# Kernel tuning notes

Hardware: AMD Instinct MI355X
Metric: run time of the kernel (lower is better)

## Reference

```python
import jax, jax.numpy as jnp
import numpy as np
from jax import lax

T, B, DX, H, DZ = 512, 64, 128, 256, 64
W_SCALE = 0.05


def setup_inputs() -> dict:
    key = jax.random.key(0)
    ks = jax.random.split(key, 16)
    r = lambda k, shape, s=W_SCALE: jax.random.normal(k, shape, dtype=jnp.float32) * s
    return {
        "X": jax.random.normal(ks[0], (T, B, DX), dtype=jnp.float32),
        "Wih_f": r(ks[1], (H, DX)), "Whh_f": r(ks[2], (H, H)),
        "bih_f": r(ks[3], (H,)), "bhh_f": r(ks[4], (H,)),
        "Wih_b": r(ks[5], (H, DX)), "Whh_b": r(ks[6], (H, H)),
        "bih_b": r(ks[7], (H,)), "bhh_b": r(ks[8], (H,)),
        "Wt": r(ks[9], (H, DZ)), "bt": r(ks[10], (H,)),
        "Wmu": r(ks[11], (DZ, H)), "bmu": r(ks[12], (DZ,)),
        "Wsig": r(ks[13], (DZ, H)), "bsig": r(ks[14], (DZ,)),
        "eps": jax.random.normal(ks[15], (T, B, DZ), dtype=jnp.float32),
    }


def _rnn_dir(X, Wih, Whh, bih, bhh):
    # Elman RNN (tanh): h_t = tanh(x_t Wih^T + bih + h_{t-1} Whh^T + bhh)
    xproj = jnp.einsum('tbd,hd->tbh', X, Wih) + bih + bhh  # big GEMM hoisted out of scan

    def step(h, xp):
        h = jnp.tanh(xp + h @ Whh.T)
        return h, h

    h0 = jnp.zeros((X.shape[1], Whh.shape[0]), dtype=X.dtype)
    _, hs = lax.scan(step, h0, xproj)
    return hs  # [T,B,H]


def reference(X, Wih_f, Whh_f, bih_f, bhh_f, Wih_b, Whh_b, bih_b, bhh_b,
              Wt, bt, Wmu, bmu, Wsig, bsig, eps):
    h_left = _rnn_dir(X, Wih_f, Whh_f, bih_f, bhh_f)
    h_right = _rnn_dir(X[::-1], Wih_b, Whh_b, bih_b, bhh_b)[::-1]

    def step(z_prev, inputs):
        hl, hr, eps_t = inputs
        tmp = jnp.tanh(z_prev @ Wt.T + bt)           # transition_net
        h_t = (tmp + hl + hr) * (1.0 / 3.0)
        mu = h_t @ Wmu.T + bmu
        std = jax.nn.softplus(h_t @ Wsig.T + bsig)
        z = mu + std * eps_t                         # reparameterization
        return z, (z, mu, std)

    z0 = jnp.zeros((X.shape[1], Wt.shape[1]), dtype=X.dtype)
    _, (z, mu, std) = lax.scan(step, z0, (h_left, h_right, eps))
    # stack outputs {z_post, mu_post, std_post} into one array [3,T,B,DZ]
    return jnp.stack([z, mu, std])
```

## Files before the change

kernel.cpp:

```cpp
#include <hip/hip_runtime.h>

#define TT 512
#define DXX 128
#define HH 256
#define DZZ 64

typedef __attribute__((ext_vector_type(8))) short short8;
typedef __attribute__((ext_vector_type(4))) float f32x4;

#define DEV static __device__ __forceinline__
#define MFMA(a,b,c) __builtin_amdgcn_mfma_f32_16x16x32_bf16((a),(b),(c),0,0,0)

DEV unsigned short f2bf(float f){
  unsigned u = __builtin_bit_cast(unsigned, f);
  u += 0x7FFFu + ((u >> 16) & 1u);
  return (unsigned short)(u >> 16);
}
DEV unsigned pack2(float lo, float hi){
  return (unsigned)f2bf(lo) | ((unsigned)f2bf(hi) << 16);
}
DEV float bfLO(unsigned u){ return __builtin_bit_cast(float, u << 16); }
DEV float bfHI(unsigned u){ return __builtin_bit_cast(float, u & 0xffff0000u); }
DEV float ftanh(float x){
  float a = fabsf(x);
  float e = __expf(-2.f * a);
  float r = __builtin_amdgcn_rcpf(1.f + e);
  float t = (1.f - e) * r;
  return copysignf(t, x);
}
DEV float fsoftplus(float x){
  float e = __expf(fminf(x, 20.f));
  float s = __logf(1.f + e);
  return (x > 20.f) ? x : s;
}
DEV void barrier_l(){
  asm volatile("s_waitcnt lgkmcnt(0)\n\ts_barrier" ::: "memory");
}


__global__ __launch_bounds__(256, 2) void phaseA(
    const float* __restrict__ X,
    const float* __restrict__ WihF, const float* __restrict__ bihF, const float* __restrict__ bhhF,
    const float* __restrict__ WihB, const float* __restrict__ bihB, const float* __restrict__ bhhB,
    unsigned short* __restrict__ xpF)
{
  const int bid = blockIdx.x;
  const int d = bid >> 9, s = bid & 511;
  const int ts = d ? (TT - 1 - s) : s;
  const float* W  = d ? WihB : WihF;
  const float* bi = d ? bihB : bihF;
  const float* bh = d ? bhhB : bhhF;

  const int tid = threadIdx.x, q = tid >> 6, l = tid & 63;
  const int l15 = l & 15, l4 = l >> 4;

  short8 wf[4][4];
  f32x4 bias[4];
  #pragma unroll
  for (int ni = 0; ni < 4; ++ni){
    int n = 64*q + 16*ni + l15;
    #pragma unroll
    for (int ks = 0; ks < 4; ++ks){
      const float* p = W + (size_t)n * DXX + ks*32 + l4*8;
      short8 v;
      #pragma unroll
      for (int i = 0; i < 8; ++i) v[i] = (short)f2bf(p[i]);
      wf[ni][ks] = v;
    }
    int n0 = 64*q + 16*ni + 4*l4;
    float4 b1 = *(const float4*)(bi + n0);
    float4 b2 = *(const float4*)(bh + n0);
    bias[ni][0]=b1.x+b2.x; bias[ni][1]=b1.y+b2.y; bias[ni][2]=b1.z+b2.z; bias[ni][3]=b1.w+b2.w;
  }

  #pragma unroll
  for (int bq = 0; bq < 4; ++bq){
    const float* xr = X + ((size_t)ts * 64 + 16*bq + l15) * DXX;
    short8 xf[4];
    #pragma unroll
    for (int ks = 0; ks < 4; ++ks){
      const float* p = xr + ks*32 + l4*8;
      short8 v;
      #pragma unroll
      for (int i = 0; i < 8; ++i) v[i] = (short)f2bf(p[i]);
      xf[ks] = v;
    }
    f32x4 acc[4];
    #pragma unroll
    for (int ni = 0; ni < 4; ++ni) acc[ni] = MFMA(wf[ni][0], xf[0], bias[ni]);
    #pragma unroll
    for (int ks = 1; ks < 4; ++ks)
      #pragma unroll
      for (int ni = 0; ni < 4; ++ni)
        acc[ni] = MFMA(wf[ni][ks], xf[ks], acc[ni]);

    unsigned wd[8];
    #pragma unroll
    for (int ni = 0; ni < 4; ++ni){
      wd[ni*2]   = pack2(acc[ni][0], acc[ni][1]);
      wd[ni*2+1] = pack2(acc[ni][2], acc[ni][3]);
    }
    unsigned short* dst = xpF + ((((size_t)d*TT + s)*4 + bq)*4 + q)*1024 + (size_t)l*16;
    uint4 o0 = {wd[0], wd[1], wd[2], wd[3]};
    uint4 o1 = {wd[4], wd[5], wd[6], wd[7]};
    ((uint4*)dst)[0] = o0;
    ((uint4*)dst)[1] = o1;
  }
}

__global__ __launch_bounds__(512, 1) void phaseB(
    const float* __restrict__ WhhF, const float* __restrict__ WhhB,
    const unsigned short* __restrict__ xpF, unsigned short* __restrict__ hF)
{
  const int dir = blockIdx.x >> 2, bq = blockIdx.x & 3;
  const float* Whh = dir ? WhhB : WhhF;
  const int tid = threadIdx.x, w = tid >> 6, l = tid & 63;
  const bool comp = (w < 4);
  const int q = w & 3;
  const int l15 = l & 15, l4 = l >> 4;
  const int swz = (l15 & 7) << 3;
  const int rbase = l15 * 256;

  __shared__ __attribute__((aligned(16))) unsigned short hbuf[2][4096];
  __shared__ __attribute__((aligned(16))) unsigned short hres[2][4096];

  short8 wf[4][8];
  if (comp){
    #pragma unroll
    for (int ni = 0; ni < 4; ++ni){
      int n = 64*q + 16*ni + l15;
      #pragma unroll
      for (int ks = 0; ks < 8; ++ks){
        const float* p = Whh + (size_t)n * HH + ks*32 + l4*8;
        short8 v;
        #pragma unroll
        for (int i = 0; i < 8; ++i) v[i] = (short)f2bf(p[i]);
        wf[ni][ks] = v;
      }
    }
  }
  for (int i = tid; i < 2048; i += 512) ((unsigned*)hbuf[0])[i] = 0u;

  const size_t strideS = 16384;
  const size_t laneOff = (size_t)bq*4096 + (size_t)q*1024 + (size_t)l*16;
  const unsigned short* xpP = xpF + (size_t)dir*TT*strideS + laneOff;
  unsigned short* hD = hF + (size_t)dir*TT*strideS + laneOff;

  uint4 xqA0, xqA1, xqB0, xqB1;
  if (comp){
    const uint4* p0 = (const uint4*)xpP;             xqA0 = p0[0]; xqA1 = p0[1];
    const uint4* p1 = (const uint4*)(xpP + strideS); xqB0 = p1[0]; xqB1 = p1[1];
  }
  __syncthreads();

  auto bstep = [&](int s, uint4& XQ0, uint4& XQ1){
    if (comp){
      const unsigned short* RD = hbuf[s & 1];
      unsigned short* WR = hbuf[(s & 1) ^ 1];
      short8 b[8];
      #pragma unroll
      for (int ks = 0; ks < 8; ++ks)
        b[ks] = *(const short8*)(RD + ((rbase + ks*32 + l4*8) ^ swz));
      f32x4 accE[4], accO[4];
      {
        unsigned W8[8] = {XQ0.x, XQ0.y, XQ0.z, XQ0.w, XQ1.x, XQ1.y, XQ1.z, XQ1.w};
        #pragma unroll
        for (int ni = 0; ni < 4; ++ni){
          accE[ni][0] = bfLO(W8[ni*2]);   accE[ni][1] = bfHI(W8[ni*2]);
          accE[ni][2] = bfLO(W8[ni*2+1]); accE[ni][3] = bfHI(W8[ni*2+1]);
          accO[ni][0] = 0.f; accO[ni][1] = 0.f; accO[ni][2] = 0.f; accO[ni][3] = 0.f;
        }
      }
      {
        int sn = (s + 2 < TT) ? s + 2 : TT - 1;
        const uint4* src = (const uint4*)(xpP + (size_t)sn * strideS);
        XQ0 = src[0]; XQ1 = src[1];
      }
      #pragma unroll
      for (int ks = 0; ks < 8; ks += 2){
        #pragma unroll
        for (int ni = 0; ni < 4; ++ni){
          accE[ni] = MFMA(wf[ni][ks],   b[ks],   accE[ni]);
          accO[ni] = MFMA(wf[ni][ks+1], b[ks+1], accO[ni]);
        }
      }
      unsigned wd[8];
      #pragma unroll
      for (int ni = 0; ni < 4; ++ni){
        float t0 = ftanh(accE[ni][0] + accO[ni][0]);
        float t1 = ftanh(accE[ni][1] + accO[ni][1]);
        float t2 = ftanh(accE[ni][2] + accO[ni][2]);
        float t3 = ftanh(accE[ni][3] + accO[ni][3]);
        unsigned lo = pack2(t0, t1), hi = pack2(t2, t3);
        wd[ni*2] = lo; wd[ni*2+1] = hi;
        int ea = rbase + ((64*q + 16*ni + 4*l4) ^ swz);
        uint2 v; v.x = lo; v.y = hi;
        *(uint2*)(WR + ea) = v;
      }
      {
        unsigned short* st = hres[s & 1] + q*1024 + l*16;
        uint4 o0 = {wd[0], wd[1], wd[2], wd[3]};
        uint4 o1 = {wd[4], wd[5], wd[6], wd[7]};
        ((uint4*)st)[0] = o0;
        ((uint4*)st)[1] = o1;
      }
    } else {
      int sg = (s > 0) ? s - 1 : 0;
      const unsigned short* src = hres[(s & 1) ^ 1] + q*1024 + l*16;
      uint4 p0 = ((const uint4*)src)[0];
      uint4 p1 = ((const uint4*)src)[1];
      size_t off = (size_t)(dir ? (TT - 1 - sg) : sg) * strideS;
      *(uint4*)(hD + off)     = p0;
      *(uint4*)(hD + off + 8) = p1;
    }
    barrier_l();
  };

  for (int s = 0; s < TT; s += 2){
    bstep(s,     xqA0, xqA1);
    bstep(s + 1, xqB0, xqB1);
  }
  if (!comp){
    const unsigned short* src = hres[1] + q*1024 + l*16;
    uint4 p0 = ((const uint4*)src)[0];
    uint4 p1 = ((const uint4*)src)[1];
    size_t off = (size_t)(dir ? 0 : (TT - 1)) * strideS;
    *(uint4*)(hD + off)     = p0;
    *(uint4*)(hD + off + 8) = p1;
  }
}

__global__ __launch_bounds__(256, 2) void phaseP(
    const float* __restrict__ Wmu, const float* __restrict__ bmu,
    const float* __restrict__ Wsig,const float* __restrict__ bsig,
    const unsigned short* __restrict__ hF, float* __restrict__ MS)
{
  const int bid = blockIdx.x;
  const int t = bid >> 2, bq = bid & 3;
  const int tid = threadIdx.x, q = tid >> 6, l = tid & 63;
  const int l15 = l & 15, l4 = l >> 4;
  const int swz = (l15 & 7) << 3;
  const int rbase = l15 * 256;

  __shared__ __attribute__((aligned(16))) unsigned short hbuf[4096];

  short8 wm[8], wsg[8];
  {
    int r = 16*q + l15;
    #pragma unroll
    for (int ks = 0; ks < 8; ++ks){
      const float* pm = Wmu  + (size_t)r * HH + ks*32 + l4*8;
      const float* ps = Wsig + (size_t)r * HH + ks*32 + l4*8;
      short8 vm, vs;
      #pragma unroll
      for (int i = 0; i < 8; ++i){
        vm[i] = (short)f2bf(pm[i] * (1.f/3.f));
        vs[i] = (short)f2bf(ps[i] * (1.f/3.f));
      }
      wm[ks] = vm; wsg[ks] = vs;
    }
  }
  f32x4 bm4, bs4;
  {
    float4 a = *(const float4*)(bmu  + 16*q + 4*l4);
    float4 b = *(const float4*)(bsig + 16*q + 4*l4);
    bm4[0]=a.x; bm4[1]=a.y; bm4[2]=a.z; bm4[3]=a.w;
    bs4[0]=b.x; bs4[1]=b.y; bs4[2]=b.z; bs4[3]=b.w;
  }

  const size_t strideS = 16384;
  const size_t laneOff = (size_t)bq*4096 + (size_t)q*1024 + (size_t)l*16;
  const unsigned short* hl = hF + (size_t)t*strideS + laneOff;
  const unsigned short* hr = hl + (size_t)TT*strideS;
  {
    uint4 a0 = ((const uint4*)hl)[0], a1 = ((const uint4*)hl)[1];
    uint4 b0 = ((const uint4*)hr)[0], b1 = ((const uint4*)hr)[1];
    unsigned HL[8] = {a0.x,a0.y,a0.z,a0.w,a1.x,a1.y,a1.z,a1.w};
    unsigned HR[8] = {b0.x,b0.y,b0.z,b0.w,b1.x,b1.y,b1.z,b1.w};
    #pragma unroll
    for (int ni = 0; ni < 4; ++ni){
      float h0 = bfLO(HL[ni*2])   + bfLO(HR[ni*2]);
      float h1 = bfHI(HL[ni*2])   + bfHI(HR[ni*2]);
      float h2 = bfLO(HL[ni*2+1]) + bfLO(HR[ni*2+1]);
      float h3 = bfHI(HL[ni*2+1]) + bfHI(HR[ni*2+1]);
      int ea = rbase + ((64*q + 16*ni + 4*l4) ^ swz);
      uint2 v; v.x = pack2(h0, h1); v.y = pack2(h2, h3);
      *(uint2*)(hbuf + ea) = v;
    }
  }
  __syncthreads();

  short8 hb[8];
  #pragma unroll
  for (int ks = 0; ks < 8; ++ks)
    hb[ks] = *(const short8*)(hbuf + ((rbase + ks*32 + l4*8) ^ swz));
  const f32x4 zero4 = {0.f,0.f,0.f,0.f};
  f32x4 am0 = MFMA(wm[0],  hb[0], bm4);
  f32x4 as0 = MFMA(wsg[0], hb[0], bs4);
  f32x4 am1 = MFMA(wm[4],  hb[4], zero4);
  f32x4 as1 = MFMA(wsg[4], hb[4], zero4);
  #pragma unroll
  for (int ks = 1; ks < 4; ++ks){
    am0 = MFMA(wm[ks],    hb[ks],   am0);
    as0 = MFMA(wsg[ks],   hb[ks],   as0);
    am1 = MFMA(wm[ks+4],  hb[ks+4], am1);
    as1 = MFMA(wsg[ks+4], hb[ks+4], as1);
  }
  f32x4 mu = am0 + am1;
  f32x4 sg = as0 + as1;
  float* dst = MS + ((((size_t)t*4 + bq)*4 + q)*64 + (size_t)l)*8;
  *(float4*)dst       = *(float4*)&mu;
  *(float4*)(dst + 4) = *(float4*)&sg;
}

__global__ __launch_bounds__(512, 1) void phaseC(
    const float* __restrict__ Wt,  const float* __restrict__ bt,
    const float* __restrict__ Wmu, const float* __restrict__ Wsig,
    const float* __restrict__ eps, const float* __restrict__ MS,
    float* __restrict__ out)
{
  const int bq = blockIdx.x;
  const int tid = threadIdx.x, w = tid >> 6, l = tid & 63;
  const bool comp = (w < 4);
  const int q = w & 3;
  const int l15 = l & 15, l4 = l >> 4;
  const int swz = (l15 & 7) << 3;
  const int rbase = l15 * 256;
  const int zrbase = l15 * 64;

  __shared__ __attribute__((aligned(16))) unsigned short zbuf[1024];
  __shared__ __attribute__((aligned(16))) unsigned short ubuf[4096];
  __shared__ __attribute__((aligned(16))) float res[3072];

  short8 wtf[4][2]; f32x4 btb[4];
  short8 wm[8], wsg[8];
  if (comp){
    #pragma unroll
    for (int ni = 0; ni < 4; ++ni){
      int n = 64*q + 16*ni + l15;
      #pragma unroll
      for (int ks = 0; ks < 2; ++ks){
        const float* p = Wt + (size_t)n * DZZ + ks*32 + l4*8;
        short8 v;
        #pragma unroll
        for (int i = 0; i < 8; ++i) v[i] = (short)f2bf(p[i]);
        wtf[ni][ks] = v;
      }
      float4 b4 = *(const float4*)(bt + 64*q + 16*ni + 4*l4);
      btb[ni][0]=b4.x; btb[ni][1]=b4.y; btb[ni][2]=b4.z; btb[ni][3]=b4.w;
    }
    int r = 16*q + l15;
    #pragma unroll
    for (int ks = 0; ks < 8; ++ks){
      const float* pm = Wmu  + (size_t)r * HH + ks*32 + l4*8;
      const float* ps = Wsig + (size_t)r * HH + ks*32 + l4*8;
      short8 vm, vs;
      #pragma unroll
      for (int i = 0; i < 8; ++i){
        vm[i] = (short)f2bf(pm[i] * (1.f/3.f));
        vs[i] = (short)f2bf(ps[i] * (1.f/3.f));
      }
      wm[ks] = vm; wsg[ks] = vs;
    }
  }
  if (tid < 512) ((unsigned*)zbuf)[tid] = 0u;

  const float* msP = MS + (((size_t)bq*4 + q)*64 + (size_t)l)*8;
  const float* eP  = eps + ((size_t)(16*bq + l15))*64 + 16*q + 4*l4;
  const int resoff = (q*64 + l)*12;
  const size_t TBZ = (size_t)TT * 64 * 64;
  const f32x4 zero4 = {0.f,0.f,0.f,0.f};

  f32x4 MPa, SPa, EFa, MPb, SPb, EFb;
  if (comp){
    float4 m0 = *(const float4*)(msP);         float4 s0 = *(const float4*)(msP + 4);
    float4 m1 = *(const float4*)(msP + 8192);  float4 s1 = *(const float4*)(msP + 8192 + 4);
    float4 e0 = *(const float4*)(eP);
    float4 e1 = *(const float4*)(eP + 4096);
    MPa[0]=m0.x;MPa[1]=m0.y;MPa[2]=m0.z;MPa[3]=m0.w;
    SPa[0]=s0.x;SPa[1]=s0.y;SPa[2]=s0.z;SPa[3]=s0.w;
    MPb[0]=m1.x;MPb[1]=m1.y;MPb[2]=m1.z;MPb[3]=m1.w;
    SPb[0]=s1.x;SPb[1]=s1.y;SPb[2]=s1.z;SPb[3]=s1.w;
    EFa[0]=e0.x;EFa[1]=e0.y;EFa[2]=e0.z;EFa[3]=e0.w;
    EFb[0]=e1.x;EFb[1]=e1.y;EFb[2]=e1.z;EFb[3]=e1.w;
  }
  __syncthreads();

  auto cstep = [&](int t, f32x4& MP, f32x4& SP, f32x4& EF){
    if (comp){
      short8 zb0 = *(const short8*)(zbuf + ((zrbase +  0 + l4*8) ^ swz));
      short8 zb1 = *(const short8*)(zbuf + ((zrbase + 32 + l4*8) ^ swz));
      f32x4 at[4];
      #pragma unroll
      for (int ni = 0; ni < 4; ++ni) at[ni] = MFMA(wtf[ni][0], zb0, btb[ni]);
      #pragma unroll
      for (int ni = 0; ni < 4; ++ni) at[ni] = MFMA(wtf[ni][1], zb1, at[ni]);
      #pragma unroll
      for (int ni = 0; ni < 4; ++ni){
        float u0 = ftanh(at[ni][0]), u1 = ftanh(at[ni][1]);
        float u2 = ftanh(at[ni][2]), u3 = ftanh(at[ni][3]);
        int ea = rbase + ((64*q + 16*ni + 4*l4) ^ swz);
        uint2 v; v.x = pack2(u0, u1); v.y = pack2(u2, u3);
        *(uint2*)(ubuf + ea) = v;
      }
    } else {
      int tp = (t > 0) ? t - 1 : 0;
      const float* rs = res + resoff;
      float4 vz = *(const float4*)(rs);
      float4 vm = *(const float4*)(rs + 4);
      float4 vs = *(const float4*)(rs + 8);
      size_t ob = ((size_t)tp*64 + 16*bq + l15)*64 + 16*q + 4*l4;
      *(float4*)(out + ob)         = vz;
      *(float4*)(out + TBZ + ob)   = vm;
      *(float4*)(out + 2*TBZ + ob) = vs;
    }
    barrier_l();

    if (comp){
      short8 hb[8];
      #pragma unroll
      for (int ks = 0; ks < 8; ++ks)
        hb[ks] = *(const short8*)(ubuf + ((rbase + ks*32 + l4*8) ^ swz));
      f32x4 am0 = MFMA(wm[0],  hb[0], MP);
      f32x4 as0 = MFMA(wsg[0], hb[0], SP);
      f32x4 am1 = MFMA(wm[4],  hb[4], zero4);
      f32x4 as1 = MFMA(wsg[4], hb[4], zero4);
      #pragma unroll
      for (int ks = 1; ks < 4; ++ks){
        am0 = MFMA(wm[ks],    hb[ks],   am0);
        as0 = MFMA(wsg[ks],   hb[ks],   as0);
        am1 = MFMA(wm[ks+4],  hb[ks+4], am1);
        as1 = MFMA(wsg[ks+4], hb[ks+4], as1);
      }
      f32x4 mu = am0 + am1;
      f32x4 sg = as0 + as1;
      f32x4 dz, dsp;
      #pragma unroll
      for (int reg = 0; reg < 4; ++reg){
        float sp = fsoftplus(sg[reg]);
        dz[reg] = __builtin_fmaf(sp, EF[reg], mu[reg]);
        dsp[reg] = sp;
      }
      {
        int zea = zrbase + ((16*q + 4*l4) ^ swz);
        uint2 v; v.x = pack2(dz[0], dz[1]); v.y = pack2(dz[2], dz[3]);
        *(uint2*)(zbuf + zea) = v;
      }
      {
        float* rw = res + resoff;
        *(float4*)(rw)     = *(float4*)&dz;
        *(float4*)(rw + 4) = *(float4*)&mu;
        *(float4*)(rw + 8) = *(float4*)&dsp;
      }
      {
        int tn = (t + 2 < TT) ? t + 2 : TT - 1;
        float4 m = *(const float4*)(msP + (size_t)tn*8192);
        float4 s = *(const float4*)(msP + (size_t)tn*8192 + 4);
        float4 e = *(const float4*)(eP + (size_t)tn*4096);
        MP[0]=m.x;MP[1]=m.y;MP[2]=m.z;MP[3]=m.w;
        SP[0]=s.x;SP[1]=s.y;SP[2]=s.z;SP[3]=s.w;
        EF[0]=e.x;EF[1]=e.y;EF[2]=e.z;EF[3]=e.w;
      }
    }
    barrier_l();
  };

  for (int t = 0; t < TT; t += 2){
    cstep(t,     MPa, SPa, EFa);
    cstep(t + 1, MPb, SPb, EFb);
  }
  if (!comp){
    const float* rs = res + resoff;
    float4 vz = *(const float4*)(rs);
    float4 vm = *(const float4*)(rs + 4);
    float4 vs = *(const float4*)(rs + 8);
    size_t ob = ((size_t)(TT-1)*64 + 16*bq + l15)*64 + 16*q + 4*l4;
    *(float4*)(out + ob)         = vz;
    *(float4*)(out + TBZ + ob)   = vm;
    *(float4*)(out + 2*TBZ + ob) = vs;
  }
}

extern "C" void kernel_launch(void* const* d_in, const int* in_sizes, int n_in,
                              void* d_out, int out_size, void* d_ws, size_t ws_size,
                              hipStream_t stream)
{
  const float* X      = (const float*)d_in[0];
  const float* Wih_f  = (const float*)d_in[1];
  const float* Whh_f  = (const float*)d_in[2];
  const float* bih_f  = (const float*)d_in[3];
  const float* bhh_f  = (const float*)d_in[4];
  const float* Wih_b  = (const float*)d_in[5];
  const float* Whh_b  = (const float*)d_in[6];
  const float* bih_b  = (const float*)d_in[7];
  const float* bhh_b  = (const float*)d_in[8];
  const float* Wt     = (const float*)d_in[9];
  const float* bt     = (const float*)d_in[10];
  const float* Wmu    = (const float*)d_in[11];
  const float* bmu    = (const float*)d_in[12];
  const float* Wsig   = (const float*)d_in[13];
  const float* bsig   = (const float*)d_in[14];
  const float* eps    = (const float*)d_in[15];

  unsigned short* xpF = (unsigned short*)d_ws;
  unsigned short* hF  = xpF + (size_t)2 * TT * 16384;
  float* MS = (float*)d_ws;

  phaseA<<<dim3(1024), dim3(256), 0, stream>>>(X, Wih_f, bih_f, bhh_f, Wih_b, bih_b, bhh_b, xpF);
  phaseB<<<dim3(8), dim3(512), 0, stream>>>(Whh_f, Whh_b, xpF, hF);
  phaseP<<<dim3(2048), dim3(256), 0, stream>>>(Wmu, bmu, Wsig, bsig, hF, MS);
  phaseC<<<dim3(4), dim3(512), 0, stream>>>(Wt, bt, Wmu, Wsig, eps, MS, (float*)d_out);
}
```

Measured before the change: 1.155 ms.

## Drop writer warps; pack two independent recurrences per block and simplify tanh

In the two serial-recurrence kernels, the dedicated writer waves are removed. Compute waves now store their results straight to global memory, and each 512-thread block runs two independent groups (the two directions in phaseB, two batch quarters in phaseC), which halves the grid size. tanh is rewritten as 1-2/(1+exp2(2x·log2e)), and bf16 packing uses the hardware-friendly __float22bfloat162_rn intrinsic. The cost is that global stores now sit on the critical path of each step, groups are coupled through shared barriers, and the new tanh form may overflow to inf for large inputs, though it still evaluates correctly.

```diff
diff --git a/kernel.cpp b/kernel.cpp
--- a/kernel.cpp
+++ b/kernel.cpp
@@ -1,4 +1,5 @@
 #include <hip/hip_runtime.h>
+#include <hip/hip_bf16.h>
 
 #define TT 512
 #define DXX 128
@@ -17,16 +18,16 @@
   return (unsigned short)(u >> 16);
 }
 DEV unsigned pack2(float lo, float hi){
-  return (unsigned)f2bf(lo) | ((unsigned)f2bf(hi) << 16);
+  __hip_bfloat162 v = __float22bfloat162_rn(float2{lo, hi});
+  unsigned r; __builtin_memcpy(&r, &v, 4);
+  return r;
 }
 DEV float bfLO(unsigned u){ return __builtin_bit_cast(float, u << 16); }
 DEV float bfHI(unsigned u){ return __builtin_bit_cast(float, u & 0xffff0000u); }
 DEV float ftanh(float x){
-  float a = fabsf(x);
-  float e = __expf(-2.f * a);
+  float e = exp2f(x * 2.885390082f);
   float r = __builtin_amdgcn_rcpf(1.f + e);
-  float t = (1.f - e) * r;
-  return copysignf(t, x);
+  return __builtin_fmaf(-2.f, r, 1.f);
 }
 DEV float fsoftplus(float x){
   float e = __expf(fminf(x, 20.f));
@@ -112,106 +113,94 @@
     const float* __restrict__ WhhF, const float* __restrict__ WhhB,
     const unsigned short* __restrict__ xpF, unsigned short* __restrict__ hF)
 {
-  const int dir = blockIdx.x >> 2, bq = blockIdx.x & 3;
+  const int bq = blockIdx.x;
+  const int tid = threadIdx.x, w = tid >> 6, l = tid & 63;
+  const int dir = w >> 2, qw = w & 3;
   const float* Whh = dir ? WhhB : WhhF;
-  const int tid = threadIdx.x, w = tid >> 6, l = tid & 63;
-  const bool comp = (w < 4);
-  const int q = w & 3;
   const int l15 = l & 15, l4 = l >> 4;
   const int swz = (l15 & 7) << 3;
   const int rbase = l15 * 256;
 
-  __shared__ __attribute__((aligned(16))) unsigned short hbuf[2][4096];
-  __shared__ __attribute__((aligned(16))) unsigned short hres[2][4096];
+  __shared__ __attribute__((aligned(16))) unsigned short hbuf[2][2][4096];
 
   short8 wf[4][8];
-  if (comp){
-    #pragma unroll
-    for (int ni = 0; ni < 4; ++ni){
-      int n = 64*q + 16*ni + l15;
-      #pragma unroll
-      for (int ks = 0; ks < 8; ++ks){
-        const float* p = Whh + (size_t)n * HH + ks*32 + l4*8;
-        short8 v;
-        #pragma unroll
-        for (int i = 0; i < 8; ++i) v[i] = (short)f2bf(p[i]);
-        wf[ni][ks] = v;
-      }
-    }
-  }
-  for (int i = tid; i < 2048; i += 512) ((unsigned*)hbuf[0])[i] = 0u;
+  #pragma unroll
+  for (int ni = 0; ni < 4; ++ni){
+    int n = 64*qw + 16*ni + l15;
+    #pragma unroll
+    for (int ks = 0; ks < 8; ++ks){
+      const float* p = Whh + (size_t)n * HH + ks*32 + l4*8;
+      short8 v;
+      #pragma unroll
+      for (int i = 0; i < 8; ++i) v[i] = (short)f2bf(p[i]);
+      wf[ni][ks] = v;
+    }
+  }
+  for (int i = tid; i < 2048; i += 512){
+    ((unsigned*)hbuf[0][0])[i] = 0u;
+    ((unsigned*)hbuf[1][0])[i] = 0u;
+  }
 
   const size_t strideS = 16384;
-  const size_t laneOff = (size_t)bq*4096 + (size_t)q*1024 + (size_t)l*16;
+  const size_t laneOff = (size_t)bq*4096 + (size_t)qw*1024 + (size_t)l*16;
   const unsigned short* xpP = xpF + (size_t)dir*TT*strideS + laneOff;
   unsigned short* hD = hF + (size_t)dir*TT*strideS + laneOff;
 
   uint4 xqA0, xqA1, xqB0, xqB1;
-  if (comp){
-    const uint4* p0 = (const uint4*)xpP;             xqA0 = p0[0]; xqA1 = p0[1];
-    const uint4* p1 = (const uint4*)(xpP + strideS); xqB0 = p1[0]; xqB1 = p1[1];
-  }
-  __syncthreads();
+  { const uint4* p = (const uint4*)xpP;             xqA0 = p[0]; xqA1 = p[1]; }
+  { const uint4* p = (const uint4*)(xpP + strideS); xqB0 = p[0]; xqB1 = p[1]; }
+
+  barrier_l();
 
   auto bstep = [&](int s, uint4& XQ0, uint4& XQ1){
-    if (comp){
-      const unsigned short* RD = hbuf[s & 1];
-      unsigned short* WR = hbuf[(s & 1) ^ 1];
-      short8 b[8];
-      #pragma unroll
-      for (int ks = 0; ks < 8; ++ks)
-        b[ks] = *(const short8*)(RD + ((rbase + ks*32 + l4*8) ^ swz));
-      f32x4 accE[4], accO[4];
-      {
-        unsigned W8[8] = {XQ0.x, XQ0.y, XQ0.z, XQ0.w, XQ1.x, XQ1.y, XQ1.z, XQ1.w};
-        #pragma unroll
-        for (int ni = 0; ni < 4; ++ni){
-          accE[ni][0] = bfLO(W8[ni*2]);   accE[ni][1] = bfHI(W8[ni*2]);
-          accE[ni][2] = bfLO(W8[ni*2+1]); accE[ni][3] = bfHI(W8[ni*2+1]);
-          accO[ni][0] = 0.f; accO[ni][1] = 0.f; accO[ni][2] = 0.f; accO[ni][3] = 0.f;
-        }
+    const unsigned short* RD = hbuf[dir][s & 1];
+    unsigned short* WR = hbuf[dir][(s & 1) ^ 1];
+    short8 b[8];
+    #pragma unroll
+    for (int ks = 0; ks < 8; ++ks)
+      b[ks] = *(const short8*)(RD + ((rbase + ks*32 + l4*8) ^ swz));
+    f32x4 accE[4], accO[4];
+    {
+      unsigned W8[8] = {XQ0.x, XQ0.y, XQ0.z, XQ0.w, XQ1.x, XQ1.y, XQ1.z, XQ1.w};
+      #pragma unroll
+      for (int ni = 0; ni < 4; ++ni){
+        accE[ni][0] = bfLO(W8[ni*2]);   accE[ni][1] = bfHI(W8[ni*2]);
+        accE[ni][2] = bfLO(W8[ni*2+1]); accE[ni][3] = bfHI(W8[ni*2+1]);
+        accO[ni][0] = 0.f; accO[ni][1] = 0.f; accO[ni][2] = 0.f; accO[ni][3] = 0.f;
       }
-      {
-        int sn = (s + 2 < TT) ? s + 2 : TT - 1;
-        const uint4* src = (const uint4*)(xpP + (size_t)sn * strideS);
-        XQ0 = src[0]; XQ1 = src[1];
+    }
+    {
+      int sn = (s + 2 < TT) ? s + 2 : TT - 1;
+      const uint4* src = (const uint4*)(xpP + (size_t)sn * strideS);
+      XQ0 = src[0]; XQ1 = src[1];
+    }
+    #pragma unroll
+    for (int ks = 0; ks < 8; ks += 2){
+      #pragma unroll
+      for (int ni = 0; ni < 4; ++ni){
+        accE[ni] = MFMA(wf[ni][ks],   b[ks],   accE[ni]);
+        accO[ni] = MFMA(wf[ni][ks+1], b[ks+1], accO[ni]);
       }
-      #pragma unroll
-      for (int ks = 0; ks < 8; ks += 2){
-        #pragma unroll
-        for (int ni = 0; ni < 4; ++ni){
-          accE[ni] = MFMA(wf[ni][ks],   b[ks],   accE[ni]);
-          accO[ni] = MFMA(wf[ni][ks+1], b[ks+1], accO[ni]);
-        }
-      }
-      unsigned wd[8];
-      #pragma unroll
-      for (int ni = 0; ni < 4; ++ni){
-        float t0 = ftanh(accE[ni][0] + accO[ni][0]);
-        float t1 = ftanh(accE[ni][1] + accO[ni][1]);
-        float t2 = ftanh(accE[ni][2] + accO[ni][2]);
-        float t3 = ftanh(accE[ni][3] + accO[ni][3]);
-        unsigned lo = pack2(t0, t1), hi = pack2(t2, t3);
-        wd[ni*2] = lo; wd[ni*2+1] = hi;
-        int ea = rbase + ((64*q + 16*ni + 4*l4) ^ swz);
-        uint2 v; v.x = lo; v.y = hi;
-        *(uint2*)(WR + ea) = v;
-      }
-      {
-        unsigned short* st = hres[s & 1] + q*1024 + l*16;
-        uint4 o0 = {wd[0], wd[1], wd[2], wd[3]};
-        uint4 o1 = {wd[4], wd[5], wd[6], wd[7]};
-        ((uint4*)st)[0] = o0;
-        ((uint4*)st)[1] = o1;
-      }
-    } else {
-      int sg = (s > 0) ? s - 1 : 0;
-      const unsigned short* src = hres[(s & 1) ^ 1] + q*1024 + l*16;
-      uint4 p0 = ((const uint4*)src)[0];
-      uint4 p1 = ((const uint4*)src)[1];
-      size_t off = (size_t)(dir ? (TT - 1 - sg) : sg) * strideS;
-      *(uint4*)(hD + off)     = p0;
-      *(uint4*)(hD + off + 8) = p1;
+    }
+    unsigned wd[8];
+    #pragma unroll
+    for (int ni = 0; ni < 4; ++ni){
+      float t0 = ftanh(accE[ni][0] + accO[ni][0]);
+      float t1 = ftanh(accE[ni][1] + accO[ni][1]);
+      float t2 = ftanh(accE[ni][2] + accO[ni][2]);
+      float t3 = ftanh(accE[ni][3] + accO[ni][3]);
+      unsigned lo = pack2(t0, t1), hi = pack2(t2, t3);
+      wd[ni*2] = lo; wd[ni*2+1] = hi;
+      int ea = rbase + ((64*qw + 16*ni + 4*l4) ^ swz);
+      uint2 v; v.x = lo; v.y = hi;
+      *(uint2*)(WR + ea) = v;
+    }
+    {
+      size_t off = (size_t)(dir ? (TT - 1 - s) : s) * strideS;
+      uint4 o0 = {wd[0], wd[1], wd[2], wd[3]};
+      uint4 o1 = {wd[4], wd[5], wd[6], wd[7]};
+      *(uint4*)(hD + off)     = o0;
+      *(uint4*)(hD + off + 8) = o1;
     }
     barrier_l();
   };
@@ -219,14 +208,6 @@
   for (int s = 0; s < TT; s += 2){
     bstep(s,     xqA0, xqA1);
     bstep(s + 1, xqB0, xqB1);
-  }
-  if (!comp){
-    const unsigned short* src = hres[1] + q*1024 + l*16;
-    uint4 p0 = ((const uint4*)src)[0];
-    uint4 p1 = ((const uint4*)src)[1];
-    size_t off = (size_t)(dir ? 0 : (TT - 1)) * strideS;
-    *(uint4*)(hD + off)     = p0;
-    *(uint4*)(hD + off + 8) = p1;
   }
 }
 
@@ -319,37 +300,35 @@
     const float* __restrict__ eps, const float* __restrict__ MS,
     float* __restrict__ out)
 {
-  const int bq = blockIdx.x;
   const int tid = threadIdx.x, w = tid >> 6, l = tid & 63;
-  const bool comp = (w < 4);
-  const int q = w & 3;
+  const int g = w >> 2, qw = w & 3;
+  const int bq = 2*blockIdx.x + g;
   const int l15 = l & 15, l4 = l >> 4;
   const int swz = (l15 & 7) << 3;
   const int rbase = l15 * 256;
   const int zrbase = l15 * 64;
 
-  __shared__ __attribute__((aligned(16))) unsigned short zbuf[1024];
-  __shared__ __attribute__((aligned(16))) unsigned short ubuf[4096];
-  __shared__ __attribute__((aligned(16))) float res[3072];
+  __shared__ __attribute__((aligned(16))) unsigned short zbuf[2][1024];
+  __shared__ __attribute__((aligned(16))) unsigned short ubuf[2][4096];
 
   short8 wtf[4][2]; f32x4 btb[4];
+  #pragma unroll
+  for (int ni = 0; ni < 4; ++ni){
+    int n = 64*qw + 16*ni + l15;
+    #pragma unroll
+    for (int ks = 0; ks < 2; ++ks){
+      const float* p = Wt + (size_t)n * DZZ + ks*32 + l4*8;
+      short8 v;
+      #pragma unroll
+      for (int i = 0; i < 8; ++i) v[i] = (short)f2bf(p[i]);
+      wtf[ni][ks] = v;
+    }
+    float4 b4 = *(const float4*)(bt + 64*qw + 16*ni + 4*l4);
+    btb[ni][0]=b4.x; btb[ni][1]=b4.y; btb[ni][2]=b4.z; btb[ni][3]=b4.w;
+  }
   short8 wm[8], wsg[8];
-  if (comp){
-    #pragma unroll
-    for (int ni = 0; ni < 4; ++ni){
-      int n = 64*q + 16*ni + l15;
-      #pragma unroll
-      for (int ks = 0; ks < 2; ++ks){
-        const float* p = Wt + (size_t)n * DZZ + ks*32 + l4*8;
-        short8 v;
-        #pragma unroll
-        for (int i = 0; i < 8; ++i) v[i] = (short)f2bf(p[i]);
-        wtf[ni][ks] = v;
-      }
-      float4 b4 = *(const float4*)(bt + 64*q + 16*ni + 4*l4);
-      btb[ni][0]=b4.x; btb[ni][1]=b4.y; btb[ni][2]=b4.z; btb[ni][3]=b4.w;
-    }
-    int r = 16*q + l15;
+  {
+    int r = 16*qw + l15;
     #pragma unroll
     for (int ks = 0; ks < 8; ++ks){
       const float* pm = Wmu  + (size_t)r * HH + ks*32 + l4*8;
@@ -363,16 +342,16 @@
       wm[ks] = vm; wsg[ks] = vs;
     }
   }
-  if (tid < 512) ((unsigned*)zbuf)[tid] = 0u;
-
-  const float* msP = MS + (((size_t)bq*4 + q)*64 + (size_t)l)*8;
-  const float* eP  = eps + ((size_t)(16*bq + l15))*64 + 16*q + 4*l4;
-  const int resoff = (q*64 + l)*12;
+  for (int i = tid; i < 1024; i += 512) ((unsigned*)zbuf)[i] = 0u;
+
+  const size_t strideS = 16384;
+  const float* msP = MS + (((size_t)bq*4 + qw)*64 + (size_t)l)*8;
+  const float* eP  = eps + ((size_t)(16*bq + l15))*64 + 16*qw + 4*l4;
   const size_t TBZ = (size_t)TT * 64 * 64;
   const f32x4 zero4 = {0.f,0.f,0.f,0.f};
 
   f32x4 MPa, SPa, EFa, MPb, SPb, EFb;
-  if (comp){
+  {
     float4 m0 = *(const float4*)(msP);         float4 s0 = *(const float4*)(msP + 4);
     float4 m1 = *(const float4*)(msP + 8192);  float4 s1 = *(const float4*)(msP + 8192 + 4);
     float4 e0 = *(const float4*)(eP);
@@ -384,83 +363,67 @@
     EFa[0]=e0.x;EFa[1]=e0.y;EFa[2]=e0.z;EFa[3]=e0.w;
     EFb[0]=e1.x;EFb[1]=e1.y;EFb[2]=e1.z;EFb[3]=e1.w;
   }
-  __syncthreads();
+  barrier_l();
 
   auto cstep = [&](int t, f32x4& MP, f32x4& SP, f32x4& EF){
-    if (comp){
-      short8 zb0 = *(const short8*)(zbuf + ((zrbase +  0 + l4*8) ^ swz));
-      short8 zb1 = *(const short8*)(zbuf + ((zrbase + 32 + l4*8) ^ swz));
-      f32x4 at[4];
-      #pragma unroll
-      for (int ni = 0; ni < 4; ++ni) at[ni] = MFMA(wtf[ni][0], zb0, btb[ni]);
-      #pragma unroll
-      for (int ni = 0; ni < 4; ++ni) at[ni] = MFMA(wtf[ni][1], zb1, at[ni]);
-      #pragma unroll
-      for (int ni = 0; ni < 4; ++ni){
-        float u0 = ftanh(at[ni][0]), u1 = ftanh(at[ni][1]);
-        float u2 = ftanh(at[ni][2]), u3 = ftanh(at[ni][3]);
-        int ea = rbase + ((64*q + 16*ni + 4*l4) ^ swz);
-        uint2 v; v.x = pack2(u0, u1); v.y = pack2(u2, u3);
-        *(uint2*)(ubuf + ea) = v;
-      }
-    } else {
-      int tp = (t > 0) ? t - 1 : 0;
-      const float* rs = res + resoff;
-      float4 vz = *(const float4*)(rs);
-      float4 vm = *(const float4*)(rs + 4);
-      float4 vs = *(const float4*)(rs + 8);
-      size_t ob = ((size_t)tp*64 + 16*bq + l15)*64 + 16*q + 4*l4;
-      *(float4*)(out + ob)         = vz;
-      *(float4*)(out + TBZ + ob)   = vm;
-      *(float4*)(out + 2*TBZ + ob) = vs;
+    short8 zb0 = *(const short8*)(zbuf[g] + ((zrbase +  0 + l4*8) ^ swz));
+    short8 zb1 = *(const short8*)(zbuf[g] + ((zrbase + 32 + l4*8) ^ swz));
+    f32x4 at[4];
+    #pragma unroll
+    for (int ni = 0; ni < 4; ++ni) at[ni] = MFMA(wtf[ni][0], zb0, btb[ni]);
+    #pragma unroll
+    for (int ni = 0; ni < 4; ++ni) at[ni] = MFMA(wtf[ni][1], zb1, at[ni]);
+    #pragma unroll
+    for (int ni = 0; ni < 4; ++ni){
+      float u0 = ftanh(at[ni][0]), u1 = ftanh(at[ni][1]);
+      float u2 = ftanh(at[ni][2]), u3 = ftanh(at[ni][3]);
+      int ea = rbase + ((64*qw + 16*ni + 4*l4) ^ swz);
+      uint2 v; v.x = pack2(u0, u1); v.y = pack2(u2, u3);
+      *(uint2*)(ubuf[g] + ea) = v;
     }
     barrier_l();
 
-    if (comp){
-      short8 hb[8];
-      #pragma unroll
-      for (int ks = 0; ks < 8; ++ks)
-        hb[ks] = *(const short8*)(ubuf + ((rbase + ks*32 + l4*8) ^ swz));
-      f32x4 am0 = MFMA(wm[0],  hb[0], MP);
-      f32x4 as0 = MFMA(wsg[0], hb[0], SP);
-      f32x4 am1 = MFMA(wm[4],  hb[4], zero4);
-      f32x4 as1 = MFMA(wsg[4], hb[4], zero4);
-      #pragma unroll
-      for (int ks = 1; ks < 4; ++ks){
-        am0 = MFMA(wm[ks],    hb[ks],   am0);
-        as0 = MFMA(wsg[ks],   hb[ks],   as0);
-        am1 = MFMA(wm[ks+4],  hb[ks+4], am1);
-        as1 = MFMA(wsg[ks+4], hb[ks+4], as1);
-      }
-      f32x4 mu = am0 + am1;
-      f32x4 sg = as0 + as1;
-      f32x4 dz, dsp;
-      #pragma unroll
-      for (int reg = 0; reg < 4; ++reg){
-        float sp = fsoftplus(sg[reg]);
-        dz[reg] = __builtin_fmaf(sp, EF[reg], mu[reg]);
-        dsp[reg] = sp;
-      }
-      {
-        int zea = zrbase + ((16*q + 4*l4) ^ swz);
-        uint2 v; v.x = pack2(dz[0], dz[1]); v.y = pack2(dz[2], dz[3]);
-        *(uint2*)(zbuf + zea) = v;
-      }
-      {
-        float* rw = res + resoff;
-        *(float4*)(rw)     = *(float4*)&dz;
-        *(float4*)(rw + 4) = *(float4*)&mu;
-        *(float4*)(rw + 8) = *(float4*)&dsp;
-      }
-      {
-        int tn = (t + 2 < TT) ? t + 2 : TT - 1;
-        float4 m = *(const float4*)(msP + (size_t)tn*8192);
-        float4 s = *(const float4*)(msP + (size_t)tn*8192 + 4);
-        float4 e = *(const float4*)(eP + (size_t)tn*4096);
-        MP[0]=m.x;MP[1]=m.y;MP[2]=m.z;MP[3]=m.w;
-        SP[0]=s.x;SP[1]=s.y;SP[2]=s.z;SP[3]=s.w;
-        EF[0]=e.x;EF[1]=e.y;EF[2]=e.z;EF[3]=e.w;
-      }
+    short8 hb[8];
+    #pragma unroll
+    for (int ks = 0; ks < 8; ++ks)
+      hb[ks] = *(const short8*)(ubuf[g] + ((rbase + ks*32 + l4*8) ^ swz));
+    f32x4 am0 = MFMA(wm[0],  hb[0], MP);
+    f32x4 as0 = MFMA(wsg[0], hb[0], SP);
+    f32x4 am1 = MFMA(wm[4],  hb[4], zero4);
+    f32x4 as1 = MFMA(wsg[4], hb[4], zero4);
+    #pragma unroll
+    for (int ks = 1; ks < 4; ++ks){
+      am0 = MFMA(wm[ks],    hb[ks],   am0);
+      as0 = MFMA(wsg[ks],   hb[ks],   as0);
+      am1 = MFMA(wm[ks+4],  hb[ks+4], am1);
+      as1 = MFMA(wsg[ks+4], hb[ks+4], as1);
+    }
+    f32x4 mu = am0 + am1;
+    f32x4 sg = as0 + as1;
+    f32x4 dz, dsp;
+    #pragma unroll
+    for (int reg = 0; reg < 4; ++reg){
+      float sp = fsoftplus(sg[reg]);
+      dz[reg]  = __builtin_fmaf(sp, EF[reg], mu[reg]);
+      dsp[reg] = sp;
+    }
+    {
+      int tn = (t + 2 < TT) ? t + 2 : TT - 1;
+      float4 m = *(const float4*)(msP + (size_t)tn*8192);
+      float4 s = *(const float4*)(msP + (size_t)tn*8192 + 4);
+      float4 e = *(const float4*)(eP + (size_t)tn*4096);
+      MP[0]=m.x;MP[1]=m.y;MP[2]=m.z;MP[3]=m.w;
+      SP[0]=s.x;SP[1]=s.y;SP[2]=s.z;SP[3]=s.w;
+      EF[0]=e.x;EF[1]=e.y;EF[2]=e.z;EF[3]=e.w;
+    }
+    {
+      int zea = zrbase + ((16*qw + 4*l4) ^ swz);
+      uint2 v; v.x = pack2(dz[0], dz[1]); v.y = pack2(dz[2], dz[3]);
+      *(uint2*)(zbuf[g] + zea) = v;
+      size_t ob = ((size_t)t*64 + 16*bq + l15)*64 + 16*qw + 4*l4;
+      *(float4*)(out + ob)         = *(float4*)&dz;
+      *(float4*)(out + TBZ + ob)   = *(float4*)&mu;
+      *(float4*)(out + 2*TBZ + ob) = *(float4*)&dsp;
     }
     barrier_l();
   };
@@ -468,16 +431,6 @@
   for (int t = 0; t < TT; t += 2){
     cstep(t,     MPa, SPa, EFa);
     cstep(t + 1, MPb, SPb, EFb);
-  }
-  if (!comp){
-    const float* rs = res + resoff;
-    float4 vz = *(const float4*)(rs);
-    float4 vm = *(const float4*)(rs + 4);
-    float4 vs = *(const float4*)(rs + 8);
-    size_t ob = ((size_t)(TT-1)*64 + 16*bq + l15)*64 + 16*q + 4*l4;
-    *(float4*)(out + ob)         = vz;
-    *(float4*)(out + TBZ + ob)   = vm;
-    *(float4*)(out + 2*TBZ + ob) = vs;
   }
 }
 
@@ -507,7 +460,7 @@
   float* MS = (float*)d_ws;
 
   phaseA<<<dim3(1024), dim3(256), 0, stream>>>(X, Wih_f, bih_f, bhh_f, Wih_b, bih_b, bhh_b, xpF);
-  phaseB<<<dim3(8), dim3(512), 0, stream>>>(Whh_f, Whh_b, xpF, hF);
+  phaseB<<<dim3(4), dim3(512), 0, stream>>>(Whh_f, Whh_b, xpF, hF);
   phaseP<<<dim3(2048), dim3(256), 0, stream>>>(Wmu, bmu, Wsig, bsig, hF, MS);
-  phaseC<<<dim3(4), dim3(512), 0, stream>>>(Wt, bt, Wmu, Wsig, eps, MS, (float*)d_out);
-}
+  phaseC<<<dim3(2), dim3(512), 0, stream>>>(Wt, bt, Wmu, Wsig, eps, MS, (float*)d_out);
+}
```

Measured after the change: 1.684 ms. +45.8%, slower.
